# Kernel optimization log

Measured on AMD Instinct MI355X. Metric: run time of the kernel, lower is better.

The kernel has to match this reference:

```python
import jax, jax.numpy as jnp
import numpy as np
import math

B, C, H, W = 4, 256, 64, 64
N_GROUPS = 32
D_K = 64
N_HEADS = C // D_K  # 4
EPS = 1e-5


def setup_inputs() -> dict:
    key = jax.random.key(0)
    ks = jax.random.split(key, 7)
    return {
        "x": jax.random.normal(ks[0], (B, C, H, W), dtype=jnp.float32),
        "gamma": jax.random.uniform(ks[1], (C,), dtype=jnp.float32),
        "beta": jax.random.normal(ks[2], (C,), dtype=jnp.float32) * 0.1,
        "W_qkv": jax.random.normal(ks[3], (C, N_HEADS * D_K * 3), dtype=jnp.float32) * 0.02,
        "b_qkv": jax.random.normal(ks[4], (N_HEADS * D_K * 3,), dtype=jnp.float32) * 0.02,
        "W_out": jax.random.normal(ks[5], (N_HEADS * D_K, C), dtype=jnp.float32) * 0.02,
        "b_out": jax.random.normal(ks[6], (C,), dtype=jnp.float32) * 0.02,
    }


def _group_norm(x, gamma, beta):
    # x: [B, C, H, W], 32 groups, biased variance, eps=1e-5 (torch GroupNorm defaults)
    b, c, h, w = x.shape
    xg = x.reshape(b, N_GROUPS, c // N_GROUPS, h, w)
    mean = jnp.mean(xg, axis=(2, 3, 4), keepdims=True)
    var = jnp.var(xg, axis=(2, 3, 4), keepdims=True)
    xn = (xg - mean) / jnp.sqrt(var + EPS)
    xn = xn.reshape(b, c, h, w)
    return xn * gamma[None, :, None, None] + beta[None, :, None, None]


def reference(x, gamma, beta, W_qkv, b_qkv, W_out, b_out):
    b, c, h, w = x.shape
    n = h * w
    scale = 1.0 / math.sqrt(math.sqrt(D_K))
    # norm -> [B, N, C]
    hid = _group_norm(x, gamma, beta).reshape(b, c, n).transpose(0, 2, 1)
    # qkv projection -> [B, N, n_heads, 3*d_k], chunk on last dim
    qkv = (hid @ W_qkv + b_qkv).reshape(b, n, N_HEADS, 3 * D_K)
    q, k, v = jnp.split(qkv, 3, axis=-1)  # each [B, N, H, d_k]
    attn = jnp.einsum('bihd,bjhd->bijh', q * scale, k * scale)
    attn = jax.nn.softmax(attn, axis=2)  # softmax over j (keys)
    res = jnp.einsum('bijh,bjhd->bihd', attn, v).reshape(b, n, N_HEADS * D_K)
    res = res @ W_out + b_out  # [B, N, C]
    res = res.transpose(0, 2, 1).reshape(b, c, h, w)
    return (res + x) / math.sqrt(2.0)
```

## Files before the change

### kernel.cpp

```cpp
#include <hip/hip_runtime.h>
#include <math.h>

typedef float  f32x4  __attribute__((ext_vector_type(4)));
typedef __bf16 bf16x8 __attribute__((ext_vector_type(8)));
typedef __bf16 bf16x4 __attribute__((ext_vector_type(4)));

#define MFMA16(a, b, c) __builtin_amdgcn_mfma_f32_16x16x32_bf16((a), (b), (c), 0, 0, 0)

#define TRR(dst, a, lit)  asm volatile("ds_read_b64_tr_b16 %0, %1 offset:" lit : "=v"(dst) : "v"(a))
#define TRRM(dst, a, lit) asm volatile("ds_read_b64_tr_b16 %0, %1 offset:" lit : "=v"(dst) : "v"(a) : "memory")
#define SHUF8(a, b) __builtin_shufflevector((a), (b), 0, 1, 2, 3, 4, 5, 6, 7)

typedef __attribute__((address_space(3))) unsigned int lds_u32;
typedef __attribute__((address_space(1))) const unsigned int glb_u32;

__device__ __forceinline__ void gload16(const __bf16* g, char* l) {
    __builtin_amdgcn_global_load_lds((glb_u32*)g, (lds_u32*)l, 16, 0, 0);
}

static constexpr int BATCH = 4;
static constexpr int CH    = 256;
static constexpr int M_TOT = BATCH * 4096;

static constexpr float QSCALE = 0.18033688011112042f;

static constexpr size_t OFF_WQKV  = 0;
static constexpr size_t OFF_WOUT  = 196608ull * 2;
static constexpr size_t OFF_STATS = OFF_WOUT + 65536ull * 2;
static constexpr size_t OFF_HID   = OFF_STATS + 1024;
static constexpr size_t OFF_Q     = OFF_HID + (size_t)M_TOT * CH * 2;
static constexpr size_t OFF_K     = OFF_Q   + (size_t)M_TOT * CH * 2;
static constexpr size_t OFF_V     = OFF_K   + (size_t)M_TOT * CH * 2;

__global__ __launch_bounds__(256) void pre_kernel(const float* __restrict__ x,
                                                  float2* __restrict__ stats,
                                                  const float* __restrict__ wq,
                                                  const float* __restrict__ wo,
                                                  __bf16* __restrict__ wqf,
                                                  __bf16* __restrict__ wof) {
    if (blockIdx.x < 128) {
        int bg = blockIdx.x;
        const float4* p = (const float4*)(x + (size_t)bg * 32768);
        float s = 0.f, ss = 0.f;
        for (int i = threadIdx.x; i < 8192; i += 256) {
            float4 v = p[i];
            s  += (v.x + v.y) + (v.z + v.w);
            ss += v.x * v.x + v.y * v.y + v.z * v.z + v.w * v.w;
        }
#pragma unroll
        for (int d = 32; d > 0; d >>= 1) { s += __shfl_down(s, d); ss += __shfl_down(ss, d); }
        __shared__ float sh[8];
        int w = threadIdx.x >> 6, l = threadIdx.x & 63;
        if (l == 0) { sh[w] = s; sh[4 + w] = ss; }
        __syncthreads();
        if (threadIdx.x == 0) {
            float S = sh[0] + sh[1] + sh[2] + sh[3];
            float SS = sh[4] + sh[5] + sh[6] + sh[7];
            float mean = S * (1.f / 32768.f);
            float var  = SS * (1.f / 32768.f) - mean * mean;
            stats[bg] = make_float2(mean, rsqrtf(var + 1e-5f));
        }
    } else {
        int i = (blockIdx.x - 128) * 256 + threadIdx.x;
        if (i < 196608) {
            int e = i & 7, l = (i >> 3) & 63, kk = (i >> 9) & 7, jt = i >> 12;
            int kidx = kk * 32 + ((l >> 4) << 3) + e;
            int n = jt * 16 + (l & 15);
            wqf[i] = (__bf16)wq[kidx * 768 + n];
        } else {
            int i2 = i - 196608;
            int e = i2 & 7, l = (i2 >> 3) & 63, kk = (i2 >> 9) & 7, jt = i2 >> 12;
            int kidx = kk * 32 + ((l >> 4) << 3) + e;
            int n = jt * 16 + (l & 15);
            wof[i2] = (__bf16)wo[kidx * 256 + n];
        }
    }
}

__global__ __launch_bounds__(256) void gn_apply(const float* __restrict__ x,
                                                const float* __restrict__ gamma,
                                                const float* __restrict__ beta,
                                                const float2* __restrict__ stats,
                                                __bf16* __restrict__ hid) {
    int b  = blockIdx.x >> 6;
    int n0 = (blockIdx.x & 63) << 6;
    int c  = threadIdx.x;
    float2 st = stats[b * 32 + (c >> 3)];
    float gm = gamma[c] * st.y;
    float bt = beta[c] - st.x * gm;
    const float* xp = x + ((size_t)(b * 256 + c)) * 4096 + n0;
    __bf16* hp = hid + ((size_t)(b * 4096 + n0)) * 256 + c;
#pragma unroll
    for (int j4 = 0; j4 < 16; ++j4) {
        float4 v = *(const float4*)(xp + j4 * 4);
        hp[(size_t)(j4 * 4 + 0) * 256] = (__bf16)(v.x * gm + bt);
        hp[(size_t)(j4 * 4 + 1) * 256] = (__bf16)(v.y * gm + bt);
        hp[(size_t)(j4 * 4 + 2) * 256] = (__bf16)(v.z * gm + bt);
        hp[(size_t)(j4 * 4 + 3) * 256] = (__bf16)(v.w * gm + bt);
    }
}

__global__ __launch_bounds__(256) void qkv_gemm(const __bf16* __restrict__ hid,
                                                const __bf16* __restrict__ wf,
                                                const float* __restrict__ bqkv,
                                                __bf16* __restrict__ qb,
                                                __bf16* __restrict__ kb,
                                                __bf16* __restrict__ vb) {
    const int mt = blockIdx.x, nt = blockIdx.y;
    const int tid = threadIdx.x;
    const int w = tid >> 6, l = tid & 63;
    const int lr = l & 15, lh = l >> 4;
    f32x4 acc[4] = {{0.f,0.f,0.f,0.f},{0.f,0.f,0.f,0.f},{0.f,0.f,0.f,0.f},{0.f,0.f,0.f,0.f}};
    const __bf16* ap = hid + (size_t)(mt * 64 + w * 16 + lr) * 256 + lh * 8;
#pragma unroll
    for (int kk = 0; kk < 8; ++kk) {
        bf16x8 a = *(const bf16x8*)(ap + kk * 32);
#pragma unroll
        for (int fj = 0; fj < 4; ++fj) {
            bf16x8 bf = *(const bf16x8*)(wf + (size_t)(((nt * 4 + fj) * 8 + kk) * 64 + l) * 8);
            acc[fj] = MFMA16(a, bf, acc[fj]);
        }
    }
    int mbase = mt * 64 + w * 16 + lh * 4;
#pragma unroll
    for (int fj = 0; fj < 4; ++fj) {
        int j = nt * 64 + fj * 16 + lr;
        int head = j / 192, rem = j % 192;
        int part = rem >> 6, dd = rem & 63;
        float bias = bqkv[j];
        float sc = (part == 0) ? QSCALE : 1.0f;
        __bf16* dst = (part == 0) ? qb : (part == 1) ? kb : vb;
#pragma unroll
        for (int r = 0; r < 4; ++r) {
            int m = mbase + r;
            int b = m >> 12, n = m & 4095;
            dst[((size_t)((b * 4 + head) * 4096 + n)) * 64 + dd] = (__bf16)((acc[fj][r] + bias) * sc);
        }
    }
}

__global__ __launch_bounds__(256, 2) void attn_fwd(const __bf16* __restrict__ q,
                                                   const __bf16* __restrict__ k,
                                                   const __bf16* __restrict__ v,
                                                   __bf16* __restrict__ ao) {
    const int id = blockIdx.x;
    const int within = id >> 3;
    const int bh = ((id & 7) << 1) + (within >> 5);
    const int q0 = (within & 31) * 128;
    const int tid = threadIdx.x;
    const int wv = tid >> 6, l = tid & 63;
    const int lr = l & 15, lh = l >> 4;

    __shared__ __attribute__((aligned(16))) char smem[32768];

    const size_t base = (size_t)bh * (4096 * 64);

    const int c0 = wv * 64 + l;
    const int rK = c0 >> 3, cbK = l & 7;
    const int gk0 = rK * 64 + (cbK ^ (rK & 7)) * 8;
    const int gk1 = gk0 + 2048;
    const int dt0 = c0 >> 7, kq0 = (c0 >> 3) & 15, klo0 = (l >> 1) & 3, d80 = l & 1;
    const int gv0 = (kq0 * 4 + klo0) * 64 + dt0 * 16 + d80 * 8;
    const int gv1 = gv0 + 32;
    const int lw0 = wv * 1024;
    const int lw1 = 4096 + wv * 1024;

    const __bf16* kg = k + base;
    const __bf16* vg = v + base;

    const unsigned vA0 = (unsigned)(size_t)(smem + 16384) + (unsigned)(lr * 2 + lh * 128);
    const unsigned vA1 = vA0 + 8192u;

    bf16x8 qf0a, qf1a, qf0b, qf1b;
    {
        const __bf16* qp = q + base + (size_t)(q0 + wv * 16 + lr) * 64 + lh * 8;
        qf0a = *(const bf16x8*)qp;
        qf1a = *(const bf16x8*)(qp + 32);
        qf0b = *(const bf16x8*)(qp + 4096);
        qf1b = *(const bf16x8*)(qp + 4096 + 32);
    }
    bf16x8 ones;
#pragma unroll
    for (int e = 0; e < 8; ++e) ones[e] = (__bf16)1.0f;

    f32x4 oa[4] = {{0.f,0.f,0.f,0.f},{0.f,0.f,0.f,0.f},{0.f,0.f,0.f,0.f},{0.f,0.f,0.f,0.f}};
    f32x4 ob[4] = {{0.f,0.f,0.f,0.f},{0.f,0.f,0.f,0.f},{0.f,0.f,0.f,0.f},{0.f,0.f,0.f,0.f}};
    f32x4 o4a = {0.f, 0.f, 0.f, 0.f};
    f32x4 o4b = {0.f, 0.f, 0.f, 0.f};

    gload16(kg + gk0, smem + lw0);
    gload16(kg + gk1, smem + lw1);
    gload16(vg + gv0, smem + 16384 + lw0);
    gload16(vg + gv1, smem + 16384 + lw1);
    __syncthreads();

    auto body = [&](const char* Kc, unsigned vA, char* kd, char* vd, int tnext) {
        if (tnext < 64) {
            const __bf16* kp = kg + (size_t)tnext * 4096;
            const __bf16* vp = vg + (size_t)tnext * 4096;
            gload16(kp + gk0, kd + lw0);
            gload16(kp + gk1, kd + lw1);
            gload16(vp + gv0, vd + lw0);
            gload16(vp + gv1, vd + lw1);
        }

        f32x4 sa[4], sb[4];
        const f32x4 z = {0.f, 0.f, 0.f, 0.f};
        __builtin_amdgcn_s_setprio(1);
#pragma unroll
        for (int fj = 0; fj < 4; ++fj) {
            int row = fj * 16 + lr;
            bf16x8 kb0 = *(const bf16x8*)(Kc + row * 128 + ((lh * 16) ^ ((row & 7) << 4)));
            bf16x8 kb1 = *(const bf16x8*)(Kc + row * 128 + (((4 + lh) * 16) ^ ((row & 7) << 4)));
            sa[fj] = MFMA16(kb0, qf0a, z);
            sb[fj] = MFMA16(kb0, qf0b, z);
            sa[fj] = MFMA16(kb1, qf1a, sa[fj]);
            sb[fj] = MFMA16(kb1, qf1b, sb[fj]);
        }
        __builtin_amdgcn_s_setprio(0);

        bf16x4 u0, u1, u2, u3, u4, u5, u6, u7, u8, u9, u10, u11, u12, u13, u14, u15;
        TRRM(u0,  vA, "0");    TRR(u1,  vA, "512");
        TRR(u2,  vA, "1024");  TRR(u3,  vA, "1536");
        TRR(u4,  vA, "2048");  TRR(u5,  vA, "2560");
        TRR(u6,  vA, "3072");  TRR(u7,  vA, "3584");
        TRR(u8,  vA, "4096");  TRR(u9,  vA, "4608");
        TRR(u10, vA, "5120");  TRR(u11, vA, "5632");
        TRR(u12, vA, "6144");  TRR(u13, vA, "6656");
        TRR(u14, vA, "7168");  TRR(u15, vA, "7680");

        bf16x8 Ba0, Ba1, Bb0, Bb1;
#pragma unroll
        for (int fj = 0; fj < 4; ++fj)
#pragma unroll
            for (int r = 0; r < 4; ++r) {
                float pa = __builtin_amdgcn_exp2f(sa[fj][r]);
                float pb = __builtin_amdgcn_exp2f(sb[fj][r]);
                if (fj < 2) { Ba0[fj * 4 + r] = (__bf16)pa; Bb0[fj * 4 + r] = (__bf16)pb; }
                else        { Ba1[(fj - 2) * 4 + r] = (__bf16)pa; Bb1[(fj - 2) * 4 + r] = (__bf16)pb; }
            }

        asm volatile("s_waitcnt lgkmcnt(0)" ::: "memory");
        __builtin_amdgcn_sched_barrier(0);
        __builtin_amdgcn_s_setprio(1);
        bf16x8 v01 = SHUF8(u0,  u1),  v23 = SHUF8(u2,  u3);
        bf16x8 v45 = SHUF8(u4,  u5),  v67 = SHUF8(u6,  u7);
        oa[0] = MFMA16(v01, Ba0, oa[0]);  ob[0] = MFMA16(v01, Bb0, ob[0]);
        oa[0] = MFMA16(v23, Ba1, oa[0]);  ob[0] = MFMA16(v23, Bb1, ob[0]);
        oa[1] = MFMA16(v45, Ba0, oa[1]);  ob[1] = MFMA16(v45, Bb0, ob[1]);
        oa[1] = MFMA16(v67, Ba1, oa[1]);  ob[1] = MFMA16(v67, Bb1, ob[1]);
        o4a   = MFMA16(ones, Ba0, o4a);   o4b   = MFMA16(ones, Bb0, o4b);
        bf16x8 v89 = SHUF8(u8,  u9),  vab = SHUF8(u10, u11);
        bf16x8 vcd = SHUF8(u12, u13), vef = SHUF8(u14, u15);
        oa[2] = MFMA16(v89, Ba0, oa[2]);  ob[2] = MFMA16(v89, Bb0, ob[2]);
        oa[2] = MFMA16(vab, Ba1, oa[2]);  ob[2] = MFMA16(vab, Bb1, ob[2]);
        oa[3] = MFMA16(vcd, Ba0, oa[3]);  ob[3] = MFMA16(vcd, Bb0, ob[3]);
        oa[3] = MFMA16(vef, Ba1, oa[3]);  ob[3] = MFMA16(vef, Bb1, ob[3]);
        o4a   = MFMA16(ones, Ba1, o4a);   o4b   = MFMA16(ones, Bb1, o4b);
        __builtin_amdgcn_s_setprio(0);

        __syncthreads();
    };

    for (int t = 0; t < 64; t += 2) {
        body(smem,        vA0, smem + 8192, smem + 16384 + 8192, t + 1);
        body(smem + 8192, vA1, smem,        smem + 16384,        t + 2);
    }

    float inva = 1.0f / o4a[0];
    float invb = 1.0f / o4b[0];
    int b = bh >> 2, h = bh & 3;
    int n = q0 + wv * 16 + lr;
    __bf16* dsta = ao + ((size_t)(b * 4096 + n)) * 256 + h * 64 + lh * 4;
    __bf16* dstb = dsta + 64 * 256;
#pragma unroll
    for (int fd = 0; fd < 4; ++fd) {
        bf16x4 pka, pkb;
#pragma unroll
        for (int r = 0; r < 4; ++r) {
            pka[r] = (__bf16)(oa[fd][r] * inva);
            pkb[r] = (__bf16)(ob[fd][r] * invb);
        }
        *(bf16x4*)(dsta + fd * 16) = pka;
        *(bf16x4*)(dstb + fd * 16) = pkb;
    }
}

__global__ __launch_bounds__(256) void out_gemm(const __bf16* __restrict__ ao,
                                                const __bf16* __restrict__ wf,
                                                const float* __restrict__ bout,
                                                const float* __restrict__ x,
                                                float* __restrict__ out) {
    const int mt = blockIdx.x, nt = blockIdx.y;
    const int tid = threadIdx.x;
    const int w = tid >> 6, l = tid & 63;
    const int lr = l & 15, lh = l >> 4;
    f32x4 acc[4] = {{0.f,0.f,0.f,0.f},{0.f,0.f,0.f,0.f},{0.f,0.f,0.f,0.f},{0.f,0.f,0.f,0.f}};
    const __bf16* ap = ao + (size_t)(mt * 64 + w * 16 + lr) * 256 + lh * 8;
#pragma unroll
    for (int kk = 0; kk < 8; ++kk) {
        bf16x8 a = *(const bf16x8*)(ap + kk * 32);
#pragma unroll
        for (int fj = 0; fj < 4; ++fj) {
            bf16x8 bf = *(const bf16x8*)(wf + (size_t)(((nt * 4 + fj) * 8 + kk) * 64 + l) * 8);
            acc[fj] = MFMA16(a, bf, acc[fj]);
        }
    }
    __shared__ float tile[64][72];
#pragma unroll
    for (int fj = 0; fj < 4; ++fj) {
        float bias = bout[nt * 64 + fj * 16 + lr];
#pragma unroll
        for (int r = 0; r < 4; ++r)
            tile[w * 16 + lh * 4 + r][fj * 16 + lr] = acc[fj][r] + bias;
    }
    __syncthreads();
    int b  = mt >> 6;
    int n0 = (mt & 63) * 64;
    int c0 = nt * 64;
    int cl = tid >> 2, nq = tid & 3;
    size_t gbase = ((size_t)(b * 256 + c0 + cl)) * 4096 + n0 + nq * 16;
#pragma unroll
    for (int i = 0; i < 16; i += 4) {
        float4 xv = *(const float4*)(x + gbase + i);
        float4 ov;
        ov.x = (tile[nq * 16 + i + 0][cl] + xv.x) * 0.70710678118654752f;
        ov.y = (tile[nq * 16 + i + 1][cl] + xv.y) * 0.70710678118654752f;
        ov.z = (tile[nq * 16 + i + 2][cl] + xv.z) * 0.70710678118654752f;
        ov.w = (tile[nq * 16 + i + 3][cl] + xv.w) * 0.70710678118654752f;
        *(float4*)(out + gbase + i) = ov;
    }
}

extern "C" void kernel_launch(void* const* d_in, const int* in_sizes, int n_in,
                              void* d_out, int out_size, void* d_ws, size_t ws_size,
                              hipStream_t stream) {
    const float* x     = (const float*)d_in[0];
    const float* gamma = (const float*)d_in[1];
    const float* beta  = (const float*)d_in[2];
    const float* W_qkv = (const float*)d_in[3];
    const float* b_qkv = (const float*)d_in[4];
    const float* W_out = (const float*)d_in[5];
    const float* b_out = (const float*)d_in[6];
    float* out = (float*)d_out;
    char* ws = (char*)d_ws;

    __bf16* wqf   = (__bf16*)(ws + OFF_WQKV);
    __bf16* wof   = (__bf16*)(ws + OFF_WOUT);
    float2* stats = (float2*)(ws + OFF_STATS);
    __bf16* hid   = (__bf16*)(ws + OFF_HID);
    __bf16* qb    = (__bf16*)(ws + OFF_Q);
    __bf16* kb    = (__bf16*)(ws + OFF_K);
    __bf16* vb    = (__bf16*)(ws + OFF_V);

    pre_kernel<<<1152, 256, 0, stream>>>(x, stats, W_qkv, W_out, wqf, wof);
    gn_apply<<<256, 256, 0, stream>>>(x, gamma, beta, stats, hid);
    qkv_gemm<<<dim3(256, 12), 256, 0, stream>>>(hid, wqf, b_qkv, qb, kb, vb);
    attn_fwd<<<512, 256, 0, stream>>>(qb, kb, vb, hid);
    out_gemm<<<dim3(256, 4), 256, 0, stream>>>(hid, wof, b_out, x, out);
}
```

Before: 137.5 us.

## Process two KV tiles per barrier phase with software-pipelined QK/PV interleave

The attention loop now loads and consumes two 64-key K/V tiles per phase, doubling shared memory to 64 KB, and double-buffers those pairs. Within a phase, the QK^T for the second tile and the V transpose reads are overlapped with exp and PV of the first tile, and MFMA order is interleaved across accumulators. The aim is to halve the barriers and hide LDS and exp latency behind matrix ops. The larger LDS footprint (64 KB per block with launch_bounds of 2 blocks) and higher register pressure could reduce occupancy.

```diff
diff --git a/kernel.cpp b/kernel.cpp
--- a/kernel.cpp
+++ b/kernel.cpp
@@ -151,7 +151,7 @@
     const int wv = tid >> 6, l = tid & 63;
     const int lr = l & 15, lh = l >> 4;
 
-    __shared__ __attribute__((aligned(16))) char smem[32768];
+    __shared__ __attribute__((aligned(16))) char smem[65536];
 
     const size_t base = (size_t)bh * (4096 * 64);
 
@@ -168,8 +168,8 @@
     const __bf16* kg = k + base;
     const __bf16* vg = v + base;
 
-    const unsigned vA0 = (unsigned)(size_t)(smem + 16384) + (unsigned)(lr * 2 + lh * 128);
-    const unsigned vA1 = vA0 + 8192u;
+    const unsigned lanep = (unsigned)(lr * 2 + lh * 128);
+    const unsigned vAbase = (unsigned)(size_t)(smem + 32768) + lanep;
 
     bf16x8 qf0a, qf1a, qf0b, qf1b;
     {
@@ -188,23 +188,7 @@
     f32x4 o4a = {0.f, 0.f, 0.f, 0.f};
     f32x4 o4b = {0.f, 0.f, 0.f, 0.f};
 
-    gload16(kg + gk0, smem + lw0);
-    gload16(kg + gk1, smem + lw1);
-    gload16(vg + gv0, smem + 16384 + lw0);
-    gload16(vg + gv1, smem + 16384 + lw1);
-    __syncthreads();
-
-    auto body = [&](const char* Kc, unsigned vA, char* kd, char* vd, int tnext) {
-        if (tnext < 64) {
-            const __bf16* kp = kg + (size_t)tnext * 4096;
-            const __bf16* vp = vg + (size_t)tnext * 4096;
-            gload16(kp + gk0, kd + lw0);
-            gload16(kp + gk1, kd + lw1);
-            gload16(vp + gv0, vd + lw0);
-            gload16(vp + gv1, vd + lw1);
-        }
-
-        f32x4 sa[4], sb[4];
+    auto qk = [&](const char* Kc, f32x4* sa, f32x4* sb) {
         const f32x4 z = {0.f, 0.f, 0.f, 0.f};
         __builtin_amdgcn_s_setprio(1);
 #pragma unroll
@@ -218,18 +202,9 @@
             sb[fj] = MFMA16(kb1, qf1b, sb[fj]);
         }
         __builtin_amdgcn_s_setprio(0);
-
-        bf16x4 u0, u1, u2, u3, u4, u5, u6, u7, u8, u9, u10, u11, u12, u13, u14, u15;
-        TRRM(u0,  vA, "0");    TRR(u1,  vA, "512");
-        TRR(u2,  vA, "1024");  TRR(u3,  vA, "1536");
-        TRR(u4,  vA, "2048");  TRR(u5,  vA, "2560");
-        TRR(u6,  vA, "3072");  TRR(u7,  vA, "3584");
-        TRR(u8,  vA, "4096");  TRR(u9,  vA, "4608");
-        TRR(u10, vA, "5120");  TRR(u11, vA, "5632");
-        TRR(u12, vA, "6144");  TRR(u13, vA, "6656");
-        TRR(u14, vA, "7168");  TRR(u15, vA, "7680");
-
-        bf16x8 Ba0, Ba1, Bb0, Bb1;
+    };
+    auto expPack = [&](const f32x4* sa, const f32x4* sb,
+                       bf16x8& Ba0, bf16x8& Ba1, bf16x8& Bb0, bf16x8& Bb1) {
 #pragma unroll
         for (int fj = 0; fj < 4; ++fj)
 #pragma unroll
@@ -239,32 +214,97 @@
                 if (fj < 2) { Ba0[fj * 4 + r] = (__bf16)pa; Bb0[fj * 4 + r] = (__bf16)pb; }
                 else        { Ba1[(fj - 2) * 4 + r] = (__bf16)pa; Bb1[(fj - 2) * 4 + r] = (__bf16)pb; }
             }
-
-        asm volatile("s_waitcnt lgkmcnt(0)" ::: "memory");
-        __builtin_amdgcn_sched_barrier(0);
+    };
+    auto pv = [&](const bf16x4* u, bf16x8 Ba0, bf16x8 Ba1, bf16x8 Bb0, bf16x8 Bb1) {
         __builtin_amdgcn_s_setprio(1);
-        bf16x8 v01 = SHUF8(u0,  u1),  v23 = SHUF8(u2,  u3);
-        bf16x8 v45 = SHUF8(u4,  u5),  v67 = SHUF8(u6,  u7);
+        bf16x8 v01 = SHUF8(u[0],  u[1]),  v23 = SHUF8(u[2],  u[3]);
+        bf16x8 v45 = SHUF8(u[4],  u[5]),  v67 = SHUF8(u[6],  u[7]);
         oa[0] = MFMA16(v01, Ba0, oa[0]);  ob[0] = MFMA16(v01, Bb0, ob[0]);
+        oa[1] = MFMA16(v45, Ba0, oa[1]);  ob[1] = MFMA16(v45, Bb0, ob[1]);
         oa[0] = MFMA16(v23, Ba1, oa[0]);  ob[0] = MFMA16(v23, Bb1, ob[0]);
-        oa[1] = MFMA16(v45, Ba0, oa[1]);  ob[1] = MFMA16(v45, Bb0, ob[1]);
         oa[1] = MFMA16(v67, Ba1, oa[1]);  ob[1] = MFMA16(v67, Bb1, ob[1]);
         o4a   = MFMA16(ones, Ba0, o4a);   o4b   = MFMA16(ones, Bb0, o4b);
-        bf16x8 v89 = SHUF8(u8,  u9),  vab = SHUF8(u10, u11);
-        bf16x8 vcd = SHUF8(u12, u13), vef = SHUF8(u14, u15);
+        bf16x8 v89 = SHUF8(u[8],  u[9]),  vab = SHUF8(u[10], u[11]);
+        bf16x8 vcd = SHUF8(u[12], u[13]), vef = SHUF8(u[14], u[15]);
         oa[2] = MFMA16(v89, Ba0, oa[2]);  ob[2] = MFMA16(v89, Bb0, ob[2]);
+        oa[3] = MFMA16(vcd, Ba0, oa[3]);  ob[3] = MFMA16(vcd, Bb0, ob[3]);
         oa[2] = MFMA16(vab, Ba1, oa[2]);  ob[2] = MFMA16(vab, Bb1, ob[2]);
-        oa[3] = MFMA16(vcd, Ba0, oa[3]);  ob[3] = MFMA16(vcd, Bb0, ob[3]);
         oa[3] = MFMA16(vef, Ba1, oa[3]);  ob[3] = MFMA16(vef, Bb1, ob[3]);
         o4a   = MFMA16(ones, Ba1, o4a);   o4b   = MFMA16(ones, Bb1, o4b);
         __builtin_amdgcn_s_setprio(0);
+    };
+
+    gload16(kg + gk0, smem + lw0);
+    gload16(kg + gk1, smem + lw1);
+    gload16(kg + 4096 + gk0, smem + 8192 + lw0);
+    gload16(kg + 4096 + gk1, smem + 8192 + lw1);
+    gload16(vg + gv0, smem + 32768 + lw0);
+    gload16(vg + gv1, smem + 32768 + lw1);
+    gload16(vg + 4096 + gv0, smem + 32768 + 8192 + lw0);
+    gload16(vg + 4096 + gv1, smem + 32768 + 8192 + lw1);
+    __syncthreads();
+
+    auto phase = [&](unsigned pb, int tnext) {
+        if (tnext < 64) {
+            const __bf16* kp = kg + (size_t)tnext * 4096;
+            const __bf16* vp = vg + (size_t)tnext * 4096;
+            char* kd = smem + (pb ^ 16384u);
+            char* vd = smem + 32768 + (pb ^ 16384u);
+            gload16(kp + gk0, kd + lw0);
+            gload16(kp + gk1, kd + lw1);
+            gload16(kp + 4096 + gk0, kd + 8192 + lw0);
+            gload16(kp + 4096 + gk1, kd + 8192 + lw1);
+            gload16(vp + gv0, vd + lw0);
+            gload16(vp + gv1, vd + lw1);
+            gload16(vp + 4096 + gv0, vd + 8192 + lw0);
+            gload16(vp + 4096 + gv1, vd + 8192 + lw1);
+        }
+        const char* Kc = smem + pb;
+        const unsigned vA = vAbase + pb;
+
+        f32x4 sa0[4], sb0[4];
+        qk(Kc, sa0, sb0);
+        bf16x4 u[16];
+        TRRM(u[0],  vA, "0");    TRR(u[1],  vA, "512");
+        TRR(u[2],  vA, "1024");  TRR(u[3],  vA, "1536");
+        TRR(u[4],  vA, "2048");  TRR(u[5],  vA, "2560");
+        TRR(u[6],  vA, "3072");  TRR(u[7],  vA, "3584");
+        TRR(u[8],  vA, "4096");  TRR(u[9],  vA, "4608");
+        TRR(u[10], vA, "5120");  TRR(u[11], vA, "5632");
+        TRR(u[12], vA, "6144");  TRR(u[13], vA, "6656");
+        TRR(u[14], vA, "7168");  TRR(u[15], vA, "7680");
+        bf16x8 Ba0, Ba1, Bb0, Bb1;
+        expPack(sa0, sb0, Ba0, Ba1, Bb0, Bb1);
+
+        f32x4 sa1[4], sb1[4];
+        qk(Kc + 8192, sa1, sb1);
+
+        asm volatile("s_waitcnt lgkmcnt(0)" ::: "memory");
+        __builtin_amdgcn_sched_barrier(0);
+        bf16x4 w[16];
+        const unsigned vA1 = vA + 8192u;
+        TRRM(w[0],  vA1, "0");    TRR(w[1],  vA1, "512");
+        TRR(w[2],  vA1, "1024");  TRR(w[3],  vA1, "1536");
+        TRR(w[4],  vA1, "2048");  TRR(w[5],  vA1, "2560");
+        TRR(w[6],  vA1, "3072");  TRR(w[7],  vA1, "3584");
+        TRR(w[8],  vA1, "4096");  TRR(w[9],  vA1, "4608");
+        TRR(w[10], vA1, "5120");  TRR(w[11], vA1, "5632");
+        TRR(w[12], vA1, "6144");  TRR(w[13], vA1, "6656");
+        TRR(w[14], vA1, "7168");  TRR(w[15], vA1, "7680");
+        pv(u, Ba0, Ba1, Bb0, Bb1);
+        bf16x8 Ca0, Ca1, Cb0, Cb1;
+        expPack(sa1, sb1, Ca0, Ca1, Cb0, Cb1);
+
+        asm volatile("s_waitcnt lgkmcnt(0)" ::: "memory");
+        __builtin_amdgcn_sched_barrier(0);
+        pv(w, Ca0, Ca1, Cb0, Cb1);
 
         __syncthreads();
     };
 
-    for (int t = 0; t < 64; t += 2) {
-        body(smem,        vA0, smem + 8192, smem + 16384 + 8192, t + 1);
-        body(smem + 8192, vA1, smem,        smem + 16384,        t + 2);
+    for (int t = 0; t < 64; t += 4) {
+        phase(0u,      t + 2);
+        phase(16384u,  t + 4);
     }
 
     float inva = 1.0f / o4a[0];
```

Result: no change. 135.0 us (median of 2 runs) (-1.8%).

## Deepen attention K/V pipeline to four LDS stages with partial vmcnt waits

Applied to the files above, without the earlier changes.

Grows the K/V shared-memory ring from two to four slots and prefetches two tiles ahead. Each iteration now waits with vmcnt(4) instead of a full __syncthreads drain, so one tile's loads stay in flight across the barrier. The PV MFMAs are also reordered to interleave independent accumulators and shorten dependency chains. LDS use doubles to 64KB per block, which may limit occupancy at two blocks per CU, and tail iterations issue redundant loads of tile 62 to keep the wait counts uniform.

```diff
diff --git a/kernel.cpp b/kernel.cpp
--- a/kernel.cpp
+++ b/kernel.cpp
@@ -151,7 +151,7 @@
     const int wv = tid >> 6, l = tid & 63;
     const int lr = l & 15, lh = l >> 4;
 
-    __shared__ __attribute__((aligned(16))) char smem[32768];
+    __shared__ __attribute__((aligned(16))) char smem[65536];
 
     const size_t base = (size_t)bh * (4096 * 64);
 
@@ -168,8 +168,8 @@
     const __bf16* kg = k + base;
     const __bf16* vg = v + base;
 
-    const unsigned vA0 = (unsigned)(size_t)(smem + 16384) + (unsigned)(lr * 2 + lh * 128);
-    const unsigned vA1 = vA0 + 8192u;
+    const unsigned lanep = (unsigned)(lr * 2 + lh * 128);
+    const unsigned vAbase = (unsigned)(size_t)(smem + 32768) + lanep;
 
     bf16x8 qf0a, qf1a, qf0b, qf1b;
     {
@@ -188,21 +188,30 @@
     f32x4 o4a = {0.f, 0.f, 0.f, 0.f};
     f32x4 o4b = {0.f, 0.f, 0.f, 0.f};
 
-    gload16(kg + gk0, smem + lw0);
-    gload16(kg + gk1, smem + lw1);
-    gload16(vg + gv0, smem + 16384 + lw0);
-    gload16(vg + gv1, smem + 16384 + lw1);
-    __syncthreads();
-
-    auto body = [&](const char* Kc, unsigned vA, char* kd, char* vd, int tnext) {
-        if (tnext < 64) {
-            const __bf16* kp = kg + (size_t)tnext * 4096;
-            const __bf16* vp = vg + (size_t)tnext * 4096;
+#pragma unroll
+    for (int s = 0; s < 2; ++s) {
+        gload16(kg + s * 4096 + gk0, smem + s * 8192 + lw0);
+        gload16(kg + s * 4096 + gk1, smem + s * 8192 + lw1);
+        gload16(vg + s * 4096 + gv0, smem + 32768 + s * 8192 + lw0);
+        gload16(vg + s * 4096 + gv1, smem + 32768 + s * 8192 + lw1);
+    }
+    asm volatile("s_waitcnt vmcnt(4)" ::: "memory");
+    __builtin_amdgcn_s_barrier();
+
+    auto body = [&](int slot, int tstage) {
+        {
+            int ts = (tstage <= 63) ? tstage : 62;
+            const __bf16* kp = kg + (size_t)ts * 4096;
+            const __bf16* vp = vg + (size_t)ts * 4096;
+            char* kd = smem + ((slot + 2) & 3) * 8192;
+            char* vd = smem + 32768 + ((slot + 2) & 3) * 8192;
             gload16(kp + gk0, kd + lw0);
             gload16(kp + gk1, kd + lw1);
             gload16(vp + gv0, vd + lw0);
             gload16(vp + gv1, vd + lw1);
         }
+        const char* Kc = smem + slot * 8192;
+        const unsigned vA = vAbase + (unsigned)(slot * 8192);
 
         f32x4 sa[4], sb[4];
         const f32x4 z = {0.f, 0.f, 0.f, 0.f};
@@ -246,25 +255,28 @@
         bf16x8 v01 = SHUF8(u0,  u1),  v23 = SHUF8(u2,  u3);
         bf16x8 v45 = SHUF8(u4,  u5),  v67 = SHUF8(u6,  u7);
         oa[0] = MFMA16(v01, Ba0, oa[0]);  ob[0] = MFMA16(v01, Bb0, ob[0]);
+        oa[1] = MFMA16(v45, Ba0, oa[1]);  ob[1] = MFMA16(v45, Bb0, ob[1]);
         oa[0] = MFMA16(v23, Ba1, oa[0]);  ob[0] = MFMA16(v23, Bb1, ob[0]);
-        oa[1] = MFMA16(v45, Ba0, oa[1]);  ob[1] = MFMA16(v45, Bb0, ob[1]);
         oa[1] = MFMA16(v67, Ba1, oa[1]);  ob[1] = MFMA16(v67, Bb1, ob[1]);
         o4a   = MFMA16(ones, Ba0, o4a);   o4b   = MFMA16(ones, Bb0, o4b);
         bf16x8 v89 = SHUF8(u8,  u9),  vab = SHUF8(u10, u11);
         bf16x8 vcd = SHUF8(u12, u13), vef = SHUF8(u14, u15);
         oa[2] = MFMA16(v89, Ba0, oa[2]);  ob[2] = MFMA16(v89, Bb0, ob[2]);
+        oa[3] = MFMA16(vcd, Ba0, oa[3]);  ob[3] = MFMA16(vcd, Bb0, ob[3]);
         oa[2] = MFMA16(vab, Ba1, oa[2]);  ob[2] = MFMA16(vab, Bb1, ob[2]);
-        oa[3] = MFMA16(vcd, Ba0, oa[3]);  ob[3] = MFMA16(vcd, Bb0, ob[3]);
         oa[3] = MFMA16(vef, Ba1, oa[3]);  ob[3] = MFMA16(vef, Bb1, ob[3]);
         o4a   = MFMA16(ones, Ba1, o4a);   o4b   = MFMA16(ones, Bb1, o4b);
         __builtin_amdgcn_s_setprio(0);
 
-        __syncthreads();
+        asm volatile("s_waitcnt vmcnt(4)" ::: "memory");
+        __builtin_amdgcn_s_barrier();
     };
 
-    for (int t = 0; t < 64; t += 2) {
-        body(smem,        vA0, smem + 8192, smem + 16384 + 8192, t + 1);
-        body(smem + 8192, vA1, smem,        smem + 16384,        t + 2);
+    for (int t = 0; t < 64; t += 4) {
+        body(0, t + 2);
+        body(1, t + 3);
+        body(2, t + 4);
+        body(3, t + 5);
     }
 
     float inva = 1.0f / o4a[0];
```

After: 137.3 us. No clear change (-0.1%).

## Pre-swizzle K into MFMA fragment layout and load K straight to registers

Applied to the files above, without the earlier changes.

The QKV GEMM now writes K through an LDS transpose tile into a fragment-major layout that matches the attention kernel's MFMA operand order. The attention kernel then loads K directly from global memory into registers, double-buffered across iterations, instead of staging it through LDS. This halves the attention kernel's shared memory and removes the K LDS reads, at the cost of more VGPRs for two 8-fragment K buffers and an extra sync and LDS tile in the GEMM. The PV MFMA issue order is also interleaved slightly differently.

```diff
diff --git a/kernel.cpp b/kernel.cpp
--- a/kernel.cpp
+++ b/kernel.cpp
@@ -104,7 +104,7 @@
                                                 const __bf16* __restrict__ wf,
                                                 const float* __restrict__ bqkv,
                                                 __bf16* __restrict__ qb,
-                                                __bf16* __restrict__ kb,
+                                                __bf16* __restrict__ kf,
                                                 __bf16* __restrict__ vb) {
     const int mt = blockIdx.x, nt = blockIdx.y;
     const int tid = threadIdx.x;
@@ -121,26 +121,53 @@
             acc[fj] = MFMA16(a, bf, acc[fj]);
         }
     }
-    int mbase = mt * 64 + w * 16 + lh * 4;
-#pragma unroll
-    for (int fj = 0; fj < 4; ++fj) {
-        int j = nt * 64 + fj * 16 + lr;
-        int head = j / 192, rem = j % 192;
-        int part = rem >> 6, dd = rem & 63;
-        float bias = bqkv[j];
-        float sc = (part == 0) ? QSCALE : 1.0f;
-        __bf16* dst = (part == 0) ? qb : (part == 1) ? kb : vb;
-#pragma unroll
-        for (int r = 0; r < 4; ++r) {
-            int m = mbase + r;
-            int b = m >> 12, n = m & 4095;
-            dst[((size_t)((b * 4 + head) * 4096 + n)) * 64 + dd] = (__bf16)((acc[fj][r] + bias) * sc);
+    const int part = nt % 3;
+    const int head = nt / 3;
+    const int b  = mt >> 6;
+    const int n0 = (mt & 63) * 64;
+
+    if (part == 1) {
+        __shared__ float tile[64][72];
+#pragma unroll
+        for (int fj = 0; fj < 4; ++fj) {
+            float bias = bqkv[head * 192 + 64 + fj * 16 + lr];
+#pragma unroll
+            for (int r = 0; r < 4; ++r)
+                tile[w * 16 + lh * 4 + r][fj * 16 + lr] = acc[fj][r] + bias;
+        }
+        __syncthreads();
+        const int f = tid >> 5;
+        const int fj2 = f & 3, half = f >> 2;
+        const int la0 = tid & 31;
+        __bf16* kdst = kf + (((size_t)((b * 4 + head) * 64 + (mt & 63)) * 8 + f) * 512);
+#pragma unroll
+        for (int s = 0; s < 2; ++s) {
+            int la = la0 + s * 32;
+            const float* src = &tile[fj2 * 16 + (la & 15)][half * 32 + ((la >> 4) & 3) * 8];
+            bf16x8 w8;
+#pragma unroll
+            for (int e = 0; e < 8; ++e) w8[e] = (__bf16)src[e];
+            *(bf16x8*)(kdst + la * 8) = w8;
+        }
+    } else {
+        __bf16* dst = (part == 0) ? qb : vb;
+        const float sc = (part == 0) ? QSCALE : 1.0f;
+        int mbase = w * 16 + lh * 4;
+#pragma unroll
+        for (int fj = 0; fj < 4; ++fj) {
+            int dd = fj * 16 + lr;
+            float bias = bqkv[head * 192 + part * 64 + dd];
+#pragma unroll
+            for (int r = 0; r < 4; ++r) {
+                int n = n0 + mbase + r;
+                dst[((size_t)((b * 4 + head) * 4096 + n)) * 64 + dd] = (__bf16)((acc[fj][r] + bias) * sc);
+            }
         }
     }
 }
 
 __global__ __launch_bounds__(256, 2) void attn_fwd(const __bf16* __restrict__ q,
-                                                   const __bf16* __restrict__ k,
+                                                   const __bf16* __restrict__ kf,
                                                    const __bf16* __restrict__ v,
                                                    __bf16* __restrict__ ao) {
     const int id = blockIdx.x;
@@ -151,25 +178,21 @@
     const int wv = tid >> 6, l = tid & 63;
     const int lr = l & 15, lh = l >> 4;
 
-    __shared__ __attribute__((aligned(16))) char smem[32768];
+    __shared__ __attribute__((aligned(16))) char smem[16384];
 
     const size_t base = (size_t)bh * (4096 * 64);
 
     const int c0 = wv * 64 + l;
-    const int rK = c0 >> 3, cbK = l & 7;
-    const int gk0 = rK * 64 + (cbK ^ (rK & 7)) * 8;
-    const int gk1 = gk0 + 2048;
     const int dt0 = c0 >> 7, kq0 = (c0 >> 3) & 15, klo0 = (l >> 1) & 3, d80 = l & 1;
     const int gv0 = (kq0 * 4 + klo0) * 64 + dt0 * 16 + d80 * 8;
     const int gv1 = gv0 + 32;
     const int lw0 = wv * 1024;
     const int lw1 = 4096 + wv * 1024;
 
-    const __bf16* kg = k + base;
     const __bf16* vg = v + base;
-
-    const unsigned vA0 = (unsigned)(size_t)(smem + 16384) + (unsigned)(lr * 2 + lh * 128);
-    const unsigned vA1 = vA0 + 8192u;
+    const __bf16* kl = kf + (size_t)bh * (64 * 4096) + l * 8;
+
+    const unsigned vAbase = (unsigned)(size_t)smem + (unsigned)(lr * 2 + lh * 128);
 
     bf16x8 qf0a, qf1a, qf0b, qf1b;
     {
@@ -188,20 +211,22 @@
     f32x4 o4a = {0.f, 0.f, 0.f, 0.f};
     f32x4 o4b = {0.f, 0.f, 0.f, 0.f};
 
-    gload16(kg + gk0, smem + lw0);
-    gload16(kg + gk1, smem + lw1);
-    gload16(vg + gv0, smem + 16384 + lw0);
-    gload16(vg + gv1, smem + 16384 + lw1);
+    gload16(vg + gv0, smem + lw0);
+    gload16(vg + gv1, smem + lw1);
+    bf16x8 kA[8], kB[8];
+#pragma unroll
+    for (int i = 0; i < 8; ++i) kA[i] = *(const bf16x8*)(kl + i * 512);
     __syncthreads();
 
-    auto body = [&](const char* Kc, unsigned vA, char* kd, char* vd, int tnext) {
+    auto body = [&](unsigned slot, bf16x8 (&kcur)[8], bf16x8 (&knext)[8], int tnext) {
         if (tnext < 64) {
-            const __bf16* kp = kg + (size_t)tnext * 4096;
             const __bf16* vp = vg + (size_t)tnext * 4096;
-            gload16(kp + gk0, kd + lw0);
-            gload16(kp + gk1, kd + lw1);
+            char* vd = smem + (slot ^ 8192u);
             gload16(vp + gv0, vd + lw0);
             gload16(vp + gv1, vd + lw1);
+            const __bf16* kp = kl + (size_t)tnext * 4096;
+#pragma unroll
+            for (int i = 0; i < 8; ++i) knext[i] = *(const bf16x8*)(kp + i * 512);
         }
 
         f32x4 sa[4], sb[4];
@@ -209,16 +234,14 @@
         __builtin_amdgcn_s_setprio(1);
 #pragma unroll
         for (int fj = 0; fj < 4; ++fj) {
-            int row = fj * 16 + lr;
-            bf16x8 kb0 = *(const bf16x8*)(Kc + row * 128 + ((lh * 16) ^ ((row & 7) << 4)));
-            bf16x8 kb1 = *(const bf16x8*)(Kc + row * 128 + (((4 + lh) * 16) ^ ((row & 7) << 4)));
-            sa[fj] = MFMA16(kb0, qf0a, z);
-            sb[fj] = MFMA16(kb0, qf0b, z);
-            sa[fj] = MFMA16(kb1, qf1a, sa[fj]);
-            sb[fj] = MFMA16(kb1, qf1b, sb[fj]);
+            sa[fj] = MFMA16(kcur[fj], qf0a, z);
+            sb[fj] = MFMA16(kcur[fj], qf0b, z);
+            sa[fj] = MFMA16(kcur[4 + fj], qf1a, sa[fj]);
+            sb[fj] = MFMA16(kcur[4 + fj], qf1b, sb[fj]);
         }
         __builtin_amdgcn_s_setprio(0);
 
+        const unsigned vA = vAbase + slot;
         bf16x4 u0, u1, u2, u3, u4, u5, u6, u7, u8, u9, u10, u11, u12, u13, u14, u15;
         TRRM(u0,  vA, "0");    TRR(u1,  vA, "512");
         TRR(u2,  vA, "1024");  TRR(u3,  vA, "1536");
@@ -246,15 +269,15 @@
         bf16x8 v01 = SHUF8(u0,  u1),  v23 = SHUF8(u2,  u3);
         bf16x8 v45 = SHUF8(u4,  u5),  v67 = SHUF8(u6,  u7);
         oa[0] = MFMA16(v01, Ba0, oa[0]);  ob[0] = MFMA16(v01, Bb0, ob[0]);
+        oa[1] = MFMA16(v45, Ba0, oa[1]);  ob[1] = MFMA16(v45, Bb0, ob[1]);
         oa[0] = MFMA16(v23, Ba1, oa[0]);  ob[0] = MFMA16(v23, Bb1, ob[0]);
-        oa[1] = MFMA16(v45, Ba0, oa[1]);  ob[1] = MFMA16(v45, Bb0, ob[1]);
         oa[1] = MFMA16(v67, Ba1, oa[1]);  ob[1] = MFMA16(v67, Bb1, ob[1]);
         o4a   = MFMA16(ones, Ba0, o4a);   o4b   = MFMA16(ones, Bb0, o4b);
         bf16x8 v89 = SHUF8(u8,  u9),  vab = SHUF8(u10, u11);
         bf16x8 vcd = SHUF8(u12, u13), vef = SHUF8(u14, u15);
         oa[2] = MFMA16(v89, Ba0, oa[2]);  ob[2] = MFMA16(v89, Bb0, ob[2]);
+        oa[3] = MFMA16(vcd, Ba0, oa[3]);  ob[3] = MFMA16(vcd, Bb0, ob[3]);
         oa[2] = MFMA16(vab, Ba1, oa[2]);  ob[2] = MFMA16(vab, Bb1, ob[2]);
-        oa[3] = MFMA16(vcd, Ba0, oa[3]);  ob[3] = MFMA16(vcd, Bb0, ob[3]);
         oa[3] = MFMA16(vef, Ba1, oa[3]);  ob[3] = MFMA16(vef, Bb1, ob[3]);
         o4a   = MFMA16(ones, Ba1, o4a);   o4b   = MFMA16(ones, Bb1, o4b);
         __builtin_amdgcn_s_setprio(0);
@@ -263,8 +286,8 @@
     };
 
     for (int t = 0; t < 64; t += 2) {
-        body(smem,        vA0, smem + 8192, smem + 16384 + 8192, t + 1);
-        body(smem + 8192, vA1, smem,        smem + 16384,        t + 2);
+        body(0u,    kA, kB, t + 1);
+        body(8192u, kB, kA, t + 2);
     }
 
     float inva = 1.0f / o4a[0];
@@ -350,12 +373,12 @@
     float2* stats = (float2*)(ws + OFF_STATS);
     __bf16* hid   = (__bf16*)(ws + OFF_HID);
     __bf16* qb    = (__bf16*)(ws + OFF_Q);
-    __bf16* kb    = (__bf16*)(ws + OFF_K);
+    __bf16* kfb   = (__bf16*)(ws + OFF_K);
     __bf16* vb    = (__bf16*)(ws + OFF_V);
 
     pre_kernel<<<1152, 256, 0, stream>>>(x, stats, W_qkv, W_out, wqf, wof);
     gn_apply<<<256, 256, 0, stream>>>(x, gamma, beta, stats, hid);
-    qkv_gemm<<<dim3(256, 12), 256, 0, stream>>>(hid, wqf, b_qkv, qb, kb, vb);
-    attn_fwd<<<512, 256, 0, stream>>>(qb, kb, vb, hid);
+    qkv_gemm<<<dim3(256, 12), 256, 0, stream>>>(hid, wqf, b_qkv, qb, kfb, vb);
+    attn_fwd<<<512, 256, 0, stream>>>(qb, kfb, vb, hid);
     out_gemm<<<dim3(256, 4), 256, 0, stream>>>(hid, wof, b_out, x, out);
 }
```

After: 141.2 us. 2.7% more time.
